# Optimization experiments

Hardware: AMD Instinct MI355X
Metric: run time of the kernel (lower is better)

Reference implementation:

```python
import jax, jax.numpy as jnp
import numpy as np

B, H, H_KV, S, D, L_MAX = 32, 32, 8, 8192, 128, 1024
GQA_GROUP = H // H_KV  # 4


def setup_inputs() -> dict:
    key = jax.random.key(0)
    k1, k2, k3, k4, k5 = jax.random.split(key, 5)
    q = jax.random.normal(k1, (B, H, 1, D), dtype=jnp.float32)
    K = jax.random.normal(k2, (B, H_KV, S, D), dtype=jnp.float32)
    V = jax.random.normal(k3, (B, H_KV, S, D), dtype=jnp.float32)
    sparse_ind = jax.random.randint(k4, (B, H, L_MAX), 0, S, dtype=jnp.int64)
    # actual lengths, kept >= 1 so the softmax denominator is never zero
    sparse_nnz = jax.random.randint(k5, (B, H), 1, L_MAX + 1, dtype=jnp.int64)
    return {"q": q, "K": K, "V": V, "sparse_ind": sparse_ind,
            "sparse_nnz": sparse_nnz, "gqa_group_size": GQA_GROUP}


def reference(q, K, V, sparse_ind, sparse_nnz, gqa_group_size):
    # q: [B,H,1,D]; K,V: [B,H_kv,S,D]; sparse_ind: [B,H,L]; sparse_nnz: [B,H]
    b, h, _, d = q.shape
    l_max = sparse_ind.shape[-1]
    scale = 1.0 / (d ** 0.5)
    kv_map = jnp.arange(h) // gqa_group_size           # [H] -> kv head id
    b_idx = jnp.arange(b)[:, None, None]               # [B,1,1]
    # gather sparse K/V rows per (batch, qo_head): [B,H,L,D]
    Kg = K[b_idx, kv_map[None, :, None], sparse_ind]
    Vg = V[b_idx, kv_map[None, :, None], sparse_ind]
    scores = jnp.einsum('bhd,bhld->bhl', q[:, :, 0, :], Kg) * scale
    valid = jnp.arange(l_max)[None, None, :] < sparse_nnz[:, :, None]
    # kernel adds -1e6 to padded positions (same effective masking)
    scores = scores + jnp.where(valid, 0.0, -1e6)
    p = jax.nn.softmax(scores, axis=-1)                # online-softmax equivalent
    out = jnp.einsum('bhl,bhld->bhd', p, Vg)
    return out[:, :, None, :]                          # [B,H,1,D]
```

## Files before the change

### kernel.cpp

```cpp
#include <hip/hip_runtime.h>
#include <math.h>

#define BB     32
#define HH     32
#define HKV    8
#define SS     8192
#define DD     128
#define LMAX   1024
#define GQA    (HH / HKV)
#define NTHR   256
#define NWAVE  4

#define CHUNK      128
#define NCHUNK     (LMAX / CHUNK)
#define RPW        (CHUNK / NWAVE)
#define WS_STRIDE  (DD + 2)

__global__ __launch_bounds__(NTHR) void sparse_attn_part(
    const float* __restrict__ q,
    const float* __restrict__ K,
    const float* __restrict__ V,
    const int*   __restrict__ ind,
    const int*   __restrict__ nnz,
    float*       __restrict__ ws)
{
    const int bh = blockIdx.x;
    const int c  = blockIdx.y;

    int L = nnz[bh];
    if (L < 1) L = 1;
    if (L > LMAX) L = LMAX;

    const int start = c * CHUNK;
    if (start >= L) return;
    const int count = min(CHUNK, L - start);

    const int b    = bh / HH;
    const int h    = bh - b * HH;
    const int kv   = h / GQA;
    const int tid  = threadIdx.x;
    const int wave = tid >> 6;
    const int lane = tid & 63;
    const int half = lane >> 5;
    const int sub  = lane & 31;

    __shared__ float s_p[CHUNK];
    __shared__ int   s_ind[CHUNK];
    __shared__ float s_red[NWAVE];
    __shared__ float s_ms[2];
    __shared__ float s_acc[NWAVE * 2][DD];

    const float* __restrict__ Kb = K + (size_t)(b * HKV + kv) * SS * DD;
    const float* __restrict__ Vb = V + (size_t)(b * HKV + kv) * SS * DD;
    const int*   __restrict__ indb = ind + (size_t)bh * LMAX + start;

    if (tid < count) s_ind[tid] = indb[tid];

    const float4 qf = *(const float4*)(q + (size_t)bh * DD + sub * 4);
    const float scale = 0.08838834764831843f;

    __syncthreads();

    const int wbeg = wave * RPW;
    const int wend = min(wbeg + RPW, count);
    #pragma unroll 4
    for (int l = wbeg + half; l < wend; l += 2) {
        const int row = s_ind[l];
        const float4 kf = *(const float4*)(Kb + (size_t)row * DD + sub * 4);
        float partial = kf.x * qf.x + kf.y * qf.y + kf.z * qf.z + kf.w * qf.w;
        #pragma unroll
        for (int off = 16; off >= 1; off >>= 1)
            partial += __shfl_xor(partial, off, 64);
        if (sub == 0) s_p[l] = partial * scale;
    }
    __syncthreads();

    float m = (tid < count) ? s_p[tid] : -INFINITY;
    #pragma unroll
    for (int off = 32; off >= 1; off >>= 1)
        m = fmaxf(m, __shfl_xor(m, off, 64));
    if (lane == 0) s_red[wave] = m;
    __syncthreads();
    m = fmaxf(fmaxf(s_red[0], s_red[1]), fmaxf(s_red[2], s_red[3]));
    __syncthreads();

    float sum = 0.f;
    if (tid < count) {
        const float p = __expf(s_p[tid] - m);
        s_p[tid] = p;
        sum = p;
    }
    #pragma unroll
    for (int off = 32; off >= 1; off >>= 1)
        sum += __shfl_xor(sum, off, 64);
    if (lane == 0) s_red[wave] = sum;
    __syncthreads();
    if (tid == 0) {
        s_ms[0] = m;
        s_ms[1] = s_red[0] + s_red[1] + s_red[2] + s_red[3];
    }

    float4 acc = make_float4(0.f, 0.f, 0.f, 0.f);
    #pragma unroll 4
    for (int l = wbeg + half; l < wend; l += 2) {
        const int row = s_ind[l];
        const float p = s_p[l];
        const float4 vf = *(const float4*)(Vb + (size_t)row * DD + sub * 4);
        acc.x = fmaf(p, vf.x, acc.x);
        acc.y = fmaf(p, vf.y, acc.y);
        acc.z = fmaf(p, vf.z, acc.z);
        acc.w = fmaf(p, vf.w, acc.w);
    }
    *(float4*)&s_acc[wave * 2 + half][sub * 4] = acc;
    __syncthreads();

    float* __restrict__ wsp = ws + ((size_t)bh * NCHUNK + c) * WS_STRIDE;
    if (tid < DD) {
        float r = 0.f;
        #pragma unroll
        for (int i = 0; i < NWAVE * 2; ++i) r += s_acc[i][tid];
        wsp[2 + tid] = r;
    } else if (tid == DD) {
        wsp[0] = s_ms[0];
    } else if (tid == DD + 1) {
        wsp[1] = s_ms[1];
    }
}

__global__ __launch_bounds__(DD) void sparse_attn_combine(
    const int*   __restrict__ nnz,
    const float* __restrict__ ws,
    float*       __restrict__ out)
{
    const int bh = blockIdx.x;
    const int t  = threadIdx.x;

    int L = nnz[bh];
    if (L < 1) L = 1;
    if (L > LMAX) L = LMAX;
    const int nc = (L + CHUNK - 1) / CHUNK;

    const float* __restrict__ base = ws + (size_t)bh * NCHUNK * WS_STRIDE;

    float M = -INFINITY;
    for (int cidx = 0; cidx < nc; ++cidx)
        M = fmaxf(M, base[cidx * WS_STRIDE]);

    float denom = 0.f, acc = 0.f;
    for (int cidx = 0; cidx < nc; ++cidx) {
        const float w = __expf(base[cidx * WS_STRIDE] - M);
        denom = fmaf(base[cidx * WS_STRIDE + 1], w, denom);
        acc   = fmaf(base[cidx * WS_STRIDE + 2 + t], w, acc);
    }
    out[(size_t)bh * DD + t] = acc / denom;
}

__global__ __launch_bounds__(NTHR) void sparse_attn_single(
    const float* __restrict__ q, const float* __restrict__ K,
    const float* __restrict__ V, const int* __restrict__ ind,
    const int* __restrict__ nnz, float* __restrict__ out)
{
    const int bh   = blockIdx.x;
    const int b    = bh / HH;
    const int h    = bh - b * HH;
    const int kv   = h / GQA;
    const int tid  = threadIdx.x;
    const int wave = tid >> 6;
    const int lane = tid & 63;

    __shared__ float s_scores[LMAX];
    __shared__ int   s_ind[LMAX];
    __shared__ float s_red[NWAVE];
    __shared__ float s_acc[NWAVE][DD];

    const float* __restrict__ Kb = K + (size_t)(b * HKV + kv) * SS * DD;
    const float* __restrict__ Vb = V + (size_t)(b * HKV + kv) * SS * DD;
    const int*   __restrict__ indb = ind + (size_t)bh * LMAX;

    int L = nnz[bh];
    if (L < 1) L = 1;
    if (L > LMAX) L = LMAX;

    for (int l = tid; l < L; l += NTHR) s_ind[l] = indb[l];
    const float2 qf = *(const float2*)(q + (size_t)bh * DD + lane * 2);
    const float scale = 0.08838834764831843f;
    __syncthreads();

    #pragma unroll 2
    for (int l = wave; l < L; l += NWAVE) {
        const int row = s_ind[l];
        const float2 kf = *(const float2*)(Kb + (size_t)row * DD + lane * 2);
        float partial = kf.x * qf.x + kf.y * qf.y;
        #pragma unroll
        for (int off = 32; off >= 1; off >>= 1)
            partial += __shfl_xor(partial, off, 64);
        if (lane == 0) s_scores[l] = partial * scale;
    }
    __syncthreads();

    float m = -INFINITY;
    for (int l = tid; l < L; l += NTHR) m = fmaxf(m, s_scores[l]);
    #pragma unroll
    for (int off = 32; off >= 1; off >>= 1)
        m = fmaxf(m, __shfl_xor(m, off, 64));
    if (lane == 0) s_red[wave] = m;
    __syncthreads();
    m = fmaxf(fmaxf(s_red[0], s_red[1]), fmaxf(s_red[2], s_red[3]));
    __syncthreads();

    float sum = 0.f;
    for (int l = tid; l < L; l += NTHR) {
        const float p = __expf(s_scores[l] - m);
        s_scores[l] = p;
        sum += p;
    }
    #pragma unroll
    for (int off = 32; off >= 1; off >>= 1)
        sum += __shfl_xor(sum, off, 64);
    if (lane == 0) s_red[wave] = sum;
    __syncthreads();
    const float inv_denom = 1.0f / (s_red[0] + s_red[1] + s_red[2] + s_red[3]);

    float accx = 0.f, accy = 0.f;
    #pragma unroll 2
    for (int l = wave; l < L; l += NWAVE) {
        const int row = s_ind[l];
        const float p = s_scores[l];
        const float2 vf = *(const float2*)(Vb + (size_t)row * DD + lane * 2);
        accx = fmaf(p, vf.x, accx);
        accy = fmaf(p, vf.y, accy);
    }
    s_acc[wave][lane * 2]     = accx;
    s_acc[wave][lane * 2 + 1] = accy;
    __syncthreads();

    if (tid < DD) {
        const float r = s_acc[0][tid] + s_acc[1][tid] + s_acc[2][tid] + s_acc[3][tid];
        out[(size_t)bh * DD + tid] = r * inv_denom;
    }
}

extern "C" void kernel_launch(void* const* d_in, const int* in_sizes, int n_in,
                              void* d_out, int out_size, void* d_ws, size_t ws_size,
                              hipStream_t stream) {
    const float* q   = (const float*)d_in[0];
    const float* K   = (const float*)d_in[1];
    const float* V   = (const float*)d_in[2];
    const int*   ind = (const int*)d_in[3];
    const int*   nnz = (const int*)d_in[4];
    float* out = (float*)d_out;

    const size_t ws_needed = (size_t)BB * HH * NCHUNK * WS_STRIDE * sizeof(float);
    if (ws_size >= ws_needed) {
        float* ws = (float*)d_ws;
        dim3 grid1(BB * HH, NCHUNK);
        sparse_attn_part<<<grid1, NTHR, 0, stream>>>(q, K, V, ind, nnz, ws);
        sparse_attn_combine<<<BB * HH, DD, 0, stream>>>(nnz, ws, out);
    } else {
        sparse_attn_single<<<BB * HH, NTHR, 0, stream>>>(q, K, V, ind, nnz, out);
    }
}
```

Measured before the change: 103.1 us.

## Fuse score and value passes into per-half-wave online softmax

Each half-wave now loads the K and V rows for an index together and keeps a running max, sum and output accumulator, rescaling whenever a larger score appears. The block-wide max and sum reductions and their barriers are gone, as is the second gather pass over the indices. A final step in shared memory merges the eight half-wave partial states with exp-weighted scaling. The goal is to remove synchronisation and put more independent K/V loads in flight per iteration. In exchange there are more exp calls, a data-dependent branch to rescale, and more live registers.

New measurement: 102.3 us. No clear change (-0.8%).

```diff
diff --git a/kernel.cpp b/kernel.cpp
--- a/kernel.cpp
+++ b/kernel.cpp
@@ -15,6 +15,7 @@
 #define NCHUNK     (LMAX / CHUNK)
 #define RPW        (CHUNK / NWAVE)
 #define WS_STRIDE  (DD + 2)
+#define NHW        (NWAVE * 2)
 
 __global__ __launch_bounds__(NTHR) void sparse_attn_part(
     const float* __restrict__ q,
@@ -43,12 +44,12 @@
     const int lane = tid & 63;
     const int half = lane >> 5;
     const int sub  = lane & 31;
-
-    __shared__ float s_p[CHUNK];
+    const int hw   = wave * 2 + half;
+
     __shared__ int   s_ind[CHUNK];
-    __shared__ float s_red[NWAVE];
-    __shared__ float s_ms[2];
-    __shared__ float s_acc[NWAVE * 2][DD];
+    __shared__ float s_m[NHW];
+    __shared__ float s_sum[NHW];
+    __shared__ float s_acc[NHW][DD];
 
     const float* __restrict__ Kb = K + (size_t)(b * HKV + kv) * SS * DD;
     const float* __restrict__ Vb = V + (size_t)(b * HKV + kv) * SS * DD;
@@ -60,6 +61,10 @@
     const float scale = 0.08838834764831843f;
 
     __syncthreads();
+
+    float  m   = -INFINITY;
+    float  sum = 0.f;
+    float4 acc = make_float4(0.f, 0.f, 0.f, 0.f);
 
     const int wbeg = wave * RPW;
     const int wend = min(wbeg + RPW, count);
@@ -67,63 +72,44 @@
     for (int l = wbeg + half; l < wend; l += 2) {
         const int row = s_ind[l];
         const float4 kf = *(const float4*)(Kb + (size_t)row * DD + sub * 4);
-        float partial = kf.x * qf.x + kf.y * qf.y + kf.z * qf.z + kf.w * qf.w;
+        const float4 vf = *(const float4*)(Vb + (size_t)row * DD + sub * 4);
+        float s = kf.x * qf.x + kf.y * qf.y + kf.z * qf.z + kf.w * qf.w;
         #pragma unroll
         for (int off = 16; off >= 1; off >>= 1)
-            partial += __shfl_xor(partial, off, 64);
-        if (sub == 0) s_p[l] = partial * scale;
-    }
-    __syncthreads();
-
-    float m = (tid < count) ? s_p[tid] : -INFINITY;
-    #pragma unroll
-    for (int off = 32; off >= 1; off >>= 1)
-        m = fmaxf(m, __shfl_xor(m, off, 64));
-    if (lane == 0) s_red[wave] = m;
-    __syncthreads();
-    m = fmaxf(fmaxf(s_red[0], s_red[1]), fmaxf(s_red[2], s_red[3]));
-    __syncthreads();
-
-    float sum = 0.f;
-    if (tid < count) {
-        const float p = __expf(s_p[tid] - m);
-        s_p[tid] = p;
-        sum = p;
-    }
-    #pragma unroll
-    for (int off = 32; off >= 1; off >>= 1)
-        sum += __shfl_xor(sum, off, 64);
-    if (lane == 0) s_red[wave] = sum;
-    __syncthreads();
-    if (tid == 0) {
-        s_ms[0] = m;
-        s_ms[1] = s_red[0] + s_red[1] + s_red[2] + s_red[3];
-    }
-
-    float4 acc = make_float4(0.f, 0.f, 0.f, 0.f);
-    #pragma unroll 4
-    for (int l = wbeg + half; l < wend; l += 2) {
-        const int row = s_ind[l];
-        const float p = s_p[l];
-        const float4 vf = *(const float4*)(Vb + (size_t)row * DD + sub * 4);
-        acc.x = fmaf(p, vf.x, acc.x);
-        acc.y = fmaf(p, vf.y, acc.y);
-        acc.z = fmaf(p, vf.z, acc.z);
-        acc.w = fmaf(p, vf.w, acc.w);
-    }
-    *(float4*)&s_acc[wave * 2 + half][sub * 4] = acc;
+            s += __shfl_xor(s, off, 64);
+        s *= scale;
+        if (s > m) {
+            const float corr = __expf(m - s);
+            acc.x *= corr; acc.y *= corr; acc.z *= corr; acc.w *= corr;
+            sum *= corr;
+            m = s;
+        }
+        const float w = __expf(s - m);
+        acc.x = fmaf(w, vf.x, acc.x);
+        acc.y = fmaf(w, vf.y, acc.y);
+        acc.z = fmaf(w, vf.z, acc.z);
+        acc.w = fmaf(w, vf.w, acc.w);
+        sum += w;
+    }
+
+    if (sub == 0) { s_m[hw] = m; s_sum[hw] = sum; }
+    *(float4*)&s_acc[hw][sub * 4] = acc;
     __syncthreads();
 
     float* __restrict__ wsp = ws + ((size_t)bh * NCHUNK + c) * WS_STRIDE;
     if (tid < DD) {
-        float r = 0.f;
-        #pragma unroll
-        for (int i = 0; i < NWAVE * 2; ++i) r += s_acc[i][tid];
+        float M = s_m[0];
+        #pragma unroll
+        for (int i = 1; i < NHW; ++i) M = fmaxf(M, s_m[i]);
+        float denom = 0.f, r = 0.f;
+        #pragma unroll
+        for (int i = 0; i < NHW; ++i) {
+            const float wgt = __expf(s_m[i] - M);
+            denom = fmaf(wgt, s_sum[i], denom);
+            r     = fmaf(wgt, s_acc[i][tid], r);
+        }
         wsp[2 + tid] = r;
-    } else if (tid == DD) {
-        wsp[0] = s_ms[0];
-    } else if (tid == DD + 1) {
-        wsp[1] = s_ms[1];
+        if (tid == 0) { wsp[0] = M; wsp[1] = denom; }
     }
 }
 
```
